# Optimization experiments

Hardware: AMD Instinct MI355X
Metric: run time of the kernel (lower is better)

The kernel has to match this reference:

```python
import math
import jax, jax.numpy as jnp
import numpy as np

B, N, D, H, PREFIX = 2, 2048, 2048, 16, 512
HD = D // H
ROPE_BASE = 10000.0

def _rope(x):
    # x: [b, h, n, d]; rotate-half RoPE with positions 0..n-1
    d = x.shape[-1]
    n = x.shape[-2]
    inv_freq = 1.0 / (ROPE_BASE ** (jnp.arange(0, d, 2, dtype=jnp.float32) / d))  # [d/2]
    pos = jnp.arange(n, dtype=jnp.float32)
    freqs = pos[:, None] * inv_freq[None, :]            # [n, d/2]
    cos, sin = jnp.cos(freqs), jnp.sin(freqs)
    x1, x2 = x[..., : d // 2], x[..., d // 2 :]
    return jnp.concatenate([x1 * cos - x2 * sin, x2 * cos + x1 * sin], axis=-1).astype(x.dtype)

def setup_inputs() -> dict:
    key = jax.random.key(0)
    ks = jax.random.split(key, 6)
    x = jax.random.normal(ks[0], (B, N, D), dtype=jnp.float32)
    prefix_k = jax.random.normal(ks[1], (B, H, PREFIX, HD), dtype=jnp.float32)
    prefix_v = jax.random.normal(ks[2], (B, H, PREFIX, HD), dtype=jnp.float32)
    Wqkv = jax.random.normal(ks[3], (D, 3 * D), dtype=jnp.float32) * (D ** -0.5)
    bqkv = jnp.zeros((3 * D,), dtype=jnp.float32)
    Wff = jax.random.normal(ks[4], (D, D), dtype=jnp.float32) * (D ** -0.5)
    bff = jnp.zeros((D,), dtype=jnp.float32)
    # causal mask over current tokens; prefix (cache) columns fully visible
    causal = jnp.tril(jnp.ones((N, N), dtype=jnp.int32))
    mask = jnp.concatenate([jnp.ones((N, PREFIX), dtype=jnp.int32), causal], axis=1)[None, None]  # [1,1,N,N+PREFIX]
    return {"x": x, "mask": mask, "prefix_k": prefix_k, "prefix_v": prefix_v,
            "Wqkv": Wqkv, "bqkv": bqkv, "Wff": Wff, "bff": bff}

def reference(x, mask, prefix_k, prefix_v, Wqkv, bqkv, Wff, bff):
    b, n, d = x.shape
    h = prefix_k.shape[1]
    hd = d // h
    qkv = (x @ Wqkv + bqkv).reshape(b, n, 3, h, hd)      # 'b n (c h d)'
    qkv = jnp.transpose(qkv, (2, 0, 3, 1, 4))            # -> c b h n d
    q, k, v = qkv[0], qkv[1], qkv[2]
    k = jnp.concatenate([prefix_k, k], axis=2)           # [b,h,kt,hd]
    v = jnp.concatenate([prefix_v, v], axis=2)
    next_prefix_kv = jnp.stack([k, v])                   # cached BEFORE rope (as in source)
    q = _rope(q)
    k = _rope(k)
    scores = jnp.einsum('bhqd,bhkd->bhqk', q, k) / math.sqrt(hd)
    scores = jnp.where(mask == 0, jnp.finfo(scores.dtype).min, scores)
    probs = jax.nn.softmax(scores, axis=-1)              # dropout_prob=0.0 -> identity
    attn_o = jnp.einsum('bhqk,bhkd->bhqd', probs, v)
    attn_o = jnp.transpose(attn_o, (0, 2, 1, 3)).reshape(b, n, d)
    return attn_o @ Wff + bff, next_prefix_kv
```

## Files before the change

kernel.cpp:

```cpp
#include <hip/hip_runtime.h>
#include <hip/hip_bf16.h>
#include <stdint.h>

#define TPB 256

using f32x4 = __attribute__((ext_vector_type(4))) float;
using s16x8 = __attribute__((ext_vector_type(8))) short;
using s16x4 = __attribute__((ext_vector_type(4))) short;

__device__ __forceinline__ short f2bf(float f){
  union { float f; uint32_t u; } v; v.f = f;
  uint32_t u = v.u;
  uint32_t r = (u + 0x7fffu + ((u >> 16) & 1u)) >> 16;
  return (short)(uint16_t)r;
}
__device__ __forceinline__ float bf2f(short b){
  union { uint32_t u; float f; } v; v.u = ((uint32_t)(uint16_t)b) << 16;
  return v.f;
}
__device__ __forceinline__ f32x4 mfma16(s16x8 a, s16x8 b, f32x4 c){
  return __builtin_amdgcn_mfma_f32_16x16x32_bf16(a, b, c, 0, 0, 0);
}

#define AS1(p) ((const __attribute__((address_space(1))) void*)(p))
#define AS3(p) ((__attribute__((address_space(3))) void*)(p))

__global__ void k_cvt_bf16(const float* __restrict__ src, short* __restrict__ dst, int n8){
  int i = blockIdx.x * TPB + threadIdx.x;
  if (i >= n8) return;
  const float4* s4 = (const float4*)src;
  float4 a = s4[2*i], b = s4[2*i+1];
  s16x8 o;
  o[0]=f2bf(a.x); o[1]=f2bf(a.y); o[2]=f2bf(a.z); o[3]=f2bf(a.w);
  o[4]=f2bf(b.x); o[5]=f2bf(b.y); o[6]=f2bf(b.z); o[7]=f2bf(b.w);
  *(s16x8*)(dst + 8*(size_t)i) = o;
}

__global__ void k_trans_cvt(const float* __restrict__ W, short* __restrict__ WT, int K, int Nn){
  __shared__ float ls[32][33];
  int k0 = blockIdx.x * 32, n0 = blockIdx.y * 32;
  int c = threadIdx.x & 31, i = threadIdx.x >> 5;
#pragma unroll
  for (int rr = 0; rr < 4; rr++){
    int row = i*4 + rr;
    ls[row][c] = W[(size_t)(k0+row)*Nn + n0 + c];
  }
  __syncthreads();
#pragma unroll
  for (int rr = 0; rr < 4; rr++){
    int ro = i*4 + rr;
    WT[(size_t)(n0+ro)*K + k0 + c] = f2bf(ls[c][ro]);
  }
}

template<int EPI>
__global__ void __launch_bounds__(512, 2) k_gemm8(
    const short* __restrict__ A, const short* __restrict__ Bt,
    int Nn, int K,
    const float* __restrict__ bias,
    float* __restrict__ outp,
    float* __restrict__ kvout,
    short* __restrict__ qpre, short* __restrict__ kpre, short* __restrict__ vpre)
{
  __shared__ __align__(16) short As[3][16384];
  __shared__ __align__(16) short Bs[3][8192];
  const int tid = threadIdx.x;
  const int w = tid >> 6, l = tid & 63;
  const int lrow = l & 15, lg = l >> 4;
  const int wm = w >> 1, wn = w & 1;
  const int m0 = blockIdx.x << 8, n0 = blockIdx.y << 7;
  const int NT = K >> 6;

  f32x4 acc[4][4] = {};

#define STAGE_A(slot, t, j) do {                                             \
    int chunk = ((w*4 + (j)) << 6) + l;                                      \
    int row = chunk >> 3, cc = chunk & 7;                                    \
    __builtin_amdgcn_global_load_lds(                                        \
      AS1(A + (size_t)(m0+row)*K + (t)*64 + ((cc ^ (row&7)) << 3)),          \
      AS3(&As[slot][(w*4 + (j)) << 9]), 16, 0, 0);                           \
  } while(0)
#define STAGE_B(slot, t, j) do {                                             \
    int chunk = ((w*2 + (j)) << 6) + l;                                      \
    int row = chunk >> 3, cc = chunk & 7;                                    \
    __builtin_amdgcn_global_load_lds(                                        \
      AS1(Bt + (size_t)(n0+row)*K + (t)*64 + ((cc ^ (row&7)) << 3)),         \
      AS3(&Bs[slot][(w*2 + (j)) << 9]), 16, 0, 0);                           \
  } while(0)

  STAGE_A(0,0,0); STAGE_A(0,0,1); STAGE_A(0,0,2); STAGE_A(0,0,3);
  STAGE_B(0,0,0); STAGE_B(0,0,1);
  STAGE_A(1,1,0); STAGE_A(1,1,1); STAGE_A(1,1,2); STAGE_A(1,1,3);
  STAGE_B(1,1,0); STAGE_B(1,1,1);

  int slot = 0;
  for (int t = 0; t < NT; ++t){
    if (t < NT-1) asm volatile("s_waitcnt vmcnt(6)" ::: "memory");
    else          asm volatile("s_waitcnt vmcnt(0)" ::: "memory");
    __builtin_amdgcn_s_barrier();
    asm volatile("" ::: "memory");
    const int sslot = (slot == 0) ? 2 : slot - 1;
    const bool st = (t+2) < NT;
    const char* ab = (const char*)As[slot];
    const char* bb = (const char*)Bs[slot];

    s16x8 bfr[4][2];
#pragma unroll
    for (int ni = 0; ni < 4; ni++){
      int row = wn*64 + ni*16 + lrow;
#pragma unroll
      for (int ks = 0; ks < 2; ks++)
        bfr[ni][ks] = *(const s16x8*)(bb + row*128 + ((ks*64 + lg*16) ^ ((row&7)<<4)));
    }
    s16x8 af[2][2];
#pragma unroll
    for (int mi = 0; mi < 2; mi++){
      int row = wm*64 + mi*16 + lrow;
#pragma unroll
      for (int ks = 0; ks < 2; ks++)
        af[mi][ks] = *(const s16x8*)(ab + row*128 + ((ks*64 + lg*16) ^ ((row&7)<<4)));
    }
    if (st){ STAGE_A(sslot,t+2,0); STAGE_A(sslot,t+2,1); STAGE_B(sslot,t+2,0); }
    __builtin_amdgcn_s_setprio(1);
#pragma unroll
    for (int ks = 0; ks < 2; ks++)
#pragma unroll
      for (int mi = 0; mi < 2; mi++)
#pragma unroll
        for (int ni = 0; ni < 4; ni++)
          acc[mi][ni] = mfma16(af[mi][ks], bfr[ni][ks], acc[mi][ni]);
    __builtin_amdgcn_s_setprio(0);
    asm volatile("" ::: "memory");
    __builtin_amdgcn_s_barrier();
    asm volatile("" ::: "memory");

    s16x8 af2[2][2];
#pragma unroll
    for (int mi = 0; mi < 2; mi++){
      int row = wm*64 + (mi+2)*16 + lrow;
#pragma unroll
      for (int ks = 0; ks < 2; ks++)
        af2[mi][ks] = *(const s16x8*)(ab + row*128 + ((ks*64 + lg*16) ^ ((row&7)<<4)));
    }
    if (st){ STAGE_A(sslot,t+2,2); STAGE_A(sslot,t+2,3); STAGE_B(sslot,t+2,1); }
    __builtin_amdgcn_s_setprio(1);
#pragma unroll
    for (int ks = 0; ks < 2; ks++)
#pragma unroll
      for (int mi = 0; mi < 2; mi++)
#pragma unroll
        for (int ni = 0; ni < 4; ni++)
          acc[mi+2][ni] = mfma16(af2[mi][ks], bfr[ni][ks], acc[mi+2][ni]);
    __builtin_amdgcn_s_setprio(0);
    slot = (slot == 2) ? 0 : slot + 1;
  }
#undef STAGE_A
#undef STAGE_B

#pragma unroll
  for (int mi = 0; mi < 4; mi++){
#pragma unroll
    for (int ni = 0; ni < 4; ni++){
      const int c  = n0 + wn*64 + ni*16 + lrow;
      const int mb = m0 + wm*64 + mi*16 + lg*4;
      const float bv = bias[c];
      if (EPI == 1){
#pragma unroll
        for (int r = 0; r < 4; r++)
          outp[(size_t)(mb+r)*Nn + c] = acc[mi][ni][r] + bv;
      } else {
        const int s = c >> 11, h = (c >> 7) & 15, tt = c & 127;
#pragma unroll
        for (int r = 0; r < 4; r++){
          const int m = mb + r;
          const int b = m >> 11, n = m & 2047;
          const int bh = b*16 + h;
          const float val = acc[mi][ni][r] + bv;
          if (s == 0){
            qpre[((size_t)bh*2048 + n)*128 + tt] = f2bf(val);
          } else if (s == 1){
            kvout[((size_t)bh*2560 + 512 + n)*128 + tt] = val;
            kpre[((size_t)bh*2048 + n)*128 + tt] = f2bf(val);
          } else {
            kvout[(size_t)(32 + bh)*327680 + (size_t)(512 + n)*128 + tt] = val;
            vpre[((size_t)bh*2048 + n)*128 + tt] = f2bf(val);
          }
        }
      }
    }
  }
}

__global__ void k_rope_k_new(const short* __restrict__ kpre, short* __restrict__ kr){
  int gid = blockIdx.x * TPB + threadIdx.x;
  int jb = (gid & 7) * 8; size_t row = gid >> 3;
  int bh = (int)(row >> 11), n = (int)(row & 2047);
  int pos = 512 + n;
  s16x8 v1 = *(const s16x8*)&kpre[row*128 + jb];
  s16x8 v2 = *(const s16x8*)&kpre[row*128 + 64 + jb];
  s16x8 o1, o2;
#pragma unroll
  for (int e = 0; e < 8; e++){
    float invf = __expf((float)(jb + e) * (-9.210340371976184f/64.0f));
    float sn, cs; __sincosf((float)pos * invf, &sn, &cs);
    float x1 = bf2f(v1[e]), x2 = bf2f(v2[e]);
    o1[e] = f2bf(x1*cs - x2*sn);
    o2[e] = f2bf(x2*cs + x1*sn);
  }
  size_t drow = (size_t)bh*2560 + pos;
  *(s16x8*)&kr[drow*128 + jb]      = o1;
  *(s16x8*)&kr[drow*128 + 64 + jb] = o2;
}

__global__ void k_rope_k_prefix(const float* __restrict__ pk, float* __restrict__ kvout0,
                                short* __restrict__ kr){
  int gid = blockIdx.x * TPB + threadIdx.x;
  int jb = (gid & 7) * 8; size_t row = gid >> 3;
  int bh = (int)(row >> 9), p = (int)(row & 511);
  float4 a1 = *(const float4*)&pk[row*128 + jb];
  float4 a2 = *(const float4*)&pk[row*128 + jb + 4];
  float4 b1 = *(const float4*)&pk[row*128 + 64 + jb];
  float4 b2 = *(const float4*)&pk[row*128 + 64 + jb + 4];
  size_t orow = (size_t)bh*2560 + p;
  *(float4*)&kvout0[orow*128 + jb]          = a1;
  *(float4*)&kvout0[orow*128 + jb + 4]      = a2;
  *(float4*)&kvout0[orow*128 + 64 + jb]     = b1;
  *(float4*)&kvout0[orow*128 + 64 + jb + 4] = b2;
  float x1[8] = {a1.x,a1.y,a1.z,a1.w,a2.x,a2.y,a2.z,a2.w};
  float x2[8] = {b1.x,b1.y,b1.z,b1.w,b2.x,b2.y,b2.z,b2.w};
  s16x8 o1, o2;
#pragma unroll
  for (int e = 0; e < 8; e++){
    float invf = __expf((float)(jb + e) * (-9.210340371976184f/64.0f));
    float sn, cs; __sincosf((float)p * invf, &sn, &cs);
    o1[e] = f2bf(x1[e]*cs - x2[e]*sn);
    o2[e] = f2bf(x2[e]*cs + x1[e]*sn);
  }
  *(s16x8*)&kr[orow*128 + jb]      = o1;
  *(s16x8*)&kr[orow*128 + 64 + jb] = o2;
}

__global__ void k_v_prefix(const float* __restrict__ pv, float* __restrict__ kvout1,
                           short* __restrict__ vT){
  __shared__ float ls[32][129];
  int bh = blockIdx.x >> 4, pt = blockIdx.x & 15;
  int p0 = pt*32, tid = threadIdx.x;
#pragma unroll
  for (int i = 0; i < 16; i++){
    int idx = i*TPB + tid; int p = idx >> 7, t = idx & 127;
    float v = pv[((size_t)bh*512 + p0 + p)*128 + t];
    ls[p][t] = v;
    kvout1[((size_t)bh*2560 + p0 + p)*128 + t] = v;
  }
  __syncthreads();
#pragma unroll
  for (int i = 0; i < 16; i++){
    int idx = i*TPB + tid; int t = idx >> 5, p = idx & 31;
    vT[((size_t)bh*128 + t)*2560 + p0 + p] = f2bf(ls[p][t]);
  }
}

__global__ void k_v_new(const short* __restrict__ vpre, short* __restrict__ vT){
  __shared__ float ls[32][129];
  int bh = blockIdx.x >> 6, nt = blockIdx.x & 63;
  int n0 = nt*32, tid = threadIdx.x;
#pragma unroll
  for (int i = 0; i < 16; i++){
    int idx = i*TPB + tid; int p = idx >> 7, t = idx & 127;
    ls[p][t] = bf2f(vpre[((size_t)bh*2048 + n0 + p)*128 + t]);
  }
  __syncthreads();
#pragma unroll
  for (int i = 0; i < 16; i++){
    int idx = i*TPB + tid; int t = idx >> 5, p = idx & 31;
    vT[((size_t)bh*128 + t)*2560 + 512 + n0 + p] = f2bf(ls[p][t]);
  }
}

__global__ void __launch_bounds__(256, 2) k_attn(
    const short* __restrict__ qr, const short* __restrict__ kr,
    const short* __restrict__ vT, short* __restrict__ attno)
{
  __shared__ short Ks[2][64*128];
  __shared__ short VTs[2][128*64];
  __shared__ short Ps[4][32*64];
  const int bh = blockIdx.x;
  const int qt = 15 - (int)blockIdx.y;
  const int n = 10 + 2*qt;
  const int tid = threadIdx.x, w = tid >> 6, l = tid & 63;
  const int lrow = l & 15, lg = l >> 4;
  const int b = bh >> 4, h = bh & 15;
  const int qbw = qt*128 + w*32;

  s16x8 qf[2][4];
  {
    const float sc = 0.088388347648318447f;
#pragma unroll
    for (int qb = 0; qb < 2; qb++){
      const int nr = qbw + qb*16 + lrow;
      const size_t rr = (size_t)bh*2048 + nr;
#pragma unroll
      for (int ks = 0; ks < 4; ks++)
        qf[qb][ks] = *(const s16x8*)&qr[rr*128 + ks*32 + lg*8];
#pragma unroll
      for (int ks = 0; ks < 2; ks++){
#pragma unroll
        for (int e = 0; e < 8; e++){
          const int j = ks*32 + lg*8 + e;
          const float invf = __expf((float)j * (-9.210340371976184f/64.0f));
          float sn, cs;
          __sincosf((float)nr * invf, &sn, &cs);
          float x1 = bf2f(qf[qb][ks][e]), x2 = bf2f(qf[qb][ks+2][e]);
          qf[qb][ks][e]   = f2bf((x1*cs - x2*sn) * sc);
          qf[qb][ks+2][e] = f2bf((x2*cs + x1*sn) * sc);
        }
      }
    }
  }

#define STAGE_KV(buf, kv0s) do {                                                    \
    _Pragma("unroll")                                                               \
    for (int i_ = 0; i_ < 4; i_++){                                                 \
      int chunk = i_*256 + tid;                                                     \
      int row = chunk >> 4, cc = (chunk & 15) ^ (row & 7);                          \
      __builtin_amdgcn_global_load_lds(                                             \
        AS1(kr + ((size_t)bh*2560 + (kv0s) + row)*128 + cc*8),                      \
        AS3((char*)Ks[buf] + (i_*256 + w*64)*16), 16, 0, 0);                        \
    }                                                                               \
    _Pragma("unroll")                                                               \
    for (int i_ = 0; i_ < 4; i_++){                                                 \
      int chunk = i_*256 + tid;                                                     \
      int row = chunk >> 3, cc = (chunk & 7) ^ (row & 7);                           \
      __builtin_amdgcn_global_load_lds(                                             \
        AS1(vT + ((size_t)bh*128 + row)*2560 + (kv0s) + cc*8),                      \
        AS3((char*)VTs[buf] + (i_*256 + w*64)*16), 16, 0, 0);                       \
    }                                                                               \
  } while(0)

  STAGE_KV(0, 0);
  STAGE_KV(1, 64);

  char* psw = (char*)&Ps[w][0];
  f32x4 acc0[8] = {}, acc1[8] = {};
  float mr0 = -1e30f, ls0 = 0.f;
  float mr1 = -1e30f, ls1 = 0.f;

  for (int t = 0; t < n; t++){
    if (t+1 < n) asm volatile("s_waitcnt vmcnt(8)" ::: "memory");
    else         asm volatile("s_waitcnt vmcnt(0)" ::: "memory");
    __builtin_amdgcn_s_barrier();
    asm volatile("" ::: "memory");
    const char* kb_ = (const char*)Ks[t&1];
    const char* vb_ = (const char*)VTs[t&1];
    const int kv0 = t*64;

    f32x4 sf0[4], sf1[4];
    __builtin_amdgcn_s_setprio(1);
#pragma unroll
    for (int kb = 0; kb < 4; kb++){
      f32x4 s0 = {0.f,0.f,0.f,0.f}, s1 = {0.f,0.f,0.f,0.f};
#pragma unroll
      for (int ks = 0; ks < 4; ks++){
        int row  = kb*16 + lrow;
        int colb = ks*64 + lg*16;
        s16x8 kf = *(const s16x8*)(kb_ + row*256 + (colb ^ ((row&7)<<4)));
        s0 = mfma16(kf, qf[0][ks], s0);
        s1 = mfma16(kf, qf[1][ks], s1);
      }
      sf0[kb] = s0; sf1[kb] = s1;
    }
    __builtin_amdgcn_s_setprio(0);

    if (kv0 + 63 > 512 + qbw){
      const int qme0 = 512 + qbw + lrow;
      const int qme1 = qme0 + 16;
#pragma unroll
      for (int kb = 0; kb < 4; kb++)
#pragma unroll
        for (int r = 0; r < 4; r++){
          int kg = kv0 + kb*16 + lg*4 + r;
          if (kg > qme0) sf0[kb][r] = -1e30f;
          if (kg > qme1) sf1[kb][r] = -1e30f;
        }
    }

    {
      float m_ = fmaxf(
          fmaxf(fmaxf(fmaxf(sf0[0][0],sf0[0][1]),fmaxf(sf0[0][2],sf0[0][3])),
                fmaxf(fmaxf(sf0[1][0],sf0[1][1]),fmaxf(sf0[1][2],sf0[1][3]))),
          fmaxf(fmaxf(fmaxf(sf0[2][0],sf0[2][1]),fmaxf(sf0[2][2],sf0[2][3])),
                fmaxf(fmaxf(sf0[3][0],sf0[3][1]),fmaxf(sf0[3][2],sf0[3][3]))));
      m_ = fmaxf(m_, __shfl_xor(m_, 16));
      m_ = fmaxf(m_, __shfl_xor(m_, 32));
      if (__any(m_ > mr0 + 8.f)){
        float mnew = fmaxf(mr0, m_);
        float sc = __expf(mr0 - mnew);
        mr0 = mnew; ls0 *= sc;
        float scr[4];
#pragma unroll
        for (int r = 0; r < 4; r++)
          scr[r] = __shfl(sc, (l & 48) | (lg*4 + r));
#pragma unroll
        for (int dt = 0; dt < 8; dt++)
#pragma unroll
          for (int r = 0; r < 4; r++) acc0[dt][r] *= scr[r];
      }
#pragma unroll
      for (int kb = 0; kb < 4; kb++){
        float p0 = __expf(sf0[kb][0] - mr0);
        float p1 = __expf(sf0[kb][1] - mr0);
        float p2 = __expf(sf0[kb][2] - mr0);
        float p3 = __expf(sf0[kb][3] - mr0);
        ls0 += (p0+p1)+(p2+p3);
        s16x4 pk4 = { f2bf(p0), f2bf(p1), f2bf(p2), f2bf(p3) };
        *(s16x4*)(psw + (lrow*128 + ((kb*32 + lg*8) ^ ((lrow&7)<<4)))) = pk4;
      }
    }
    {
      float m_ = fmaxf(
          fmaxf(fmaxf(fmaxf(sf1[0][0],sf1[0][1]),fmaxf(sf1[0][2],sf1[0][3])),
                fmaxf(fmaxf(sf1[1][0],sf1[1][1]),fmaxf(sf1[1][2],sf1[1][3]))),
          fmaxf(fmaxf(fmaxf(sf1[2][0],sf1[2][1]),fmaxf(sf1[2][2],sf1[2][3])),
                fmaxf(fmaxf(sf1[3][0],sf1[3][1]),fmaxf(sf1[3][2],sf1[3][3]))));
      m_ = fmaxf(m_, __shfl_xor(m_, 16));
      m_ = fmaxf(m_, __shfl_xor(m_, 32));
      if (__any(m_ > mr1 + 8.f)){
        float mnew = fmaxf(mr1, m_);
        float sc = __expf(mr1 - mnew);
        mr1 = mnew; ls1 *= sc;
        float scr[4];
#pragma unroll
        for (int r = 0; r < 4; r++)
          scr[r] = __shfl(sc, (l & 48) | (lg*4 + r));
#pragma unroll
        for (int dt = 0; dt < 8; dt++)
#pragma unroll
          for (int r = 0; r < 4; r++) acc1[dt][r] *= scr[r];
      }
#pragma unroll
      for (int kb = 0; kb < 4; kb++){
        float p0 = __expf(sf1[kb][0] - mr1);
        float p1 = __expf(sf1[kb][1] - mr1);
        float p2 = __expf(sf1[kb][2] - mr1);
        float p3 = __expf(sf1[kb][3] - mr1);
        ls1 += (p0+p1)+(p2+p3);
        s16x4 pk4 = { f2bf(p0), f2bf(p1), f2bf(p2), f2bf(p3) };
        *(s16x4*)(psw + ((16 + lrow)*128 + ((kb*32 + lg*8) ^ ((lrow&7)<<4)))) = pk4;
      }
    }

    __builtin_amdgcn_s_setprio(1);
#pragma unroll
    for (int kp = 0; kp < 2; kp++){
      s16x8 pa0 = *(const s16x8*)(psw + (lrow*128       + ((kp*64 + lg*16) ^ ((lrow&7)<<4))));
      s16x8 pa1 = *(const s16x8*)(psw + ((16+lrow)*128  + ((kp*64 + lg*16) ^ ((lrow&7)<<4))));
#pragma unroll
      for (int dt = 0; dt < 8; dt++){
        int vrow = dt*16 + lrow;
        int vcolb = kp*64 + lg*16;
        s16x8 vf = *(const s16x8*)(vb_ + vrow*128 + (vcolb ^ ((vrow&7)<<4)));
        acc0[dt] = mfma16(pa0, vf, acc0[dt]);
        acc1[dt] = mfma16(pa1, vf, acc1[dt]);
      }
    }
    __builtin_amdgcn_s_setprio(0);

    asm volatile("" ::: "memory");
    __builtin_amdgcn_s_barrier();
    asm volatile("" ::: "memory");
    if (t + 2 < n) STAGE_KV(t&1, (t+2)*64);
  }

  float lsa = ls0;
  lsa += __shfl_xor(lsa, 16);
  lsa += __shfl_xor(lsa, 32);
  float lsb = ls1;
  lsb += __shfl_xor(lsb, 16);
  lsb += __shfl_xor(lsb, 32);
  float linv0[4], linv1[4];
#pragma unroll
  for (int r = 0; r < 4; r++){
    linv0[r] = 1.f / __shfl(lsa, (l & 48) | (lg*4 + r));
    linv1[r] = 1.f / __shfl(lsb, (l & 48) | (lg*4 + r));
  }
#pragma unroll
  for (int dt = 0; dt < 8; dt++){
#pragma unroll
    for (int r = 0; r < 4; r++){
      const int dcol = h*128 + dt*16 + lrow;
      const int nrow0 = qbw + lg*4 + r;
      const int nrow1 = qbw + 16 + lg*4 + r;
      attno[((size_t)b*2048 + nrow0)*2048 + dcol] = f2bf(acc0[dt][r] * linv0[r]);
      attno[((size_t)b*2048 + nrow1)*2048 + dcol] = f2bf(acc1[dt][r] * linv1[r]);
    }
  }
#undef STAGE_KV
}

extern "C" void kernel_launch(void* const* d_in, const int* in_sizes, int n_in,
                              void* d_out, int out_size, void* d_ws, size_t ws_size,
                              hipStream_t stream)
{
  const float* x    = (const float*)d_in[0];
  const float* pk   = (const float*)d_in[2];
  const float* pv   = (const float*)d_in[3];
  const float* Wqkv = (const float*)d_in[4];
  const float* bqkv = (const float*)d_in[5];
  const float* Wff  = (const float*)d_in[6];
  const float* bff  = (const float*)d_in[7];
  float* out   = (float*)d_out;
  float* kvout = out + 8388608;

  char* ws = (char*)d_ws;
  short* xb    = (short*)(ws);
  short* wqkvT = (short*)(ws + 16777216);
  short* wffT  = (short*)(ws + 41943040);
  short* qpre  = (short*)(ws + 50331648);
  short* kpre  = (short*)(ws + 67108864);
  short* vpre  = (short*)(ws + 83886080);
  short* krp   = (short*)(ws + 117440512);
  short* vTp   = (short*)(ws + 138412032);
  short* attno = (short*)(ws + 159383552);

  k_cvt_bf16<<<4096, TPB, 0, stream>>>(x, xb, 1048576);
  k_trans_cvt<<<dim3(64, 192), TPB, 0, stream>>>(Wqkv, wqkvT, 2048, 6144);
  k_trans_cvt<<<dim3(64, 64),  TPB, 0, stream>>>(Wff,  wffT,  2048, 2048);

  k_gemm8<0><<<dim3(16, 48), 512, 0, stream>>>(xb, wqkvT, 6144, 2048, bqkv,
                                               nullptr, kvout, qpre, kpre, vpre);

  k_rope_k_new<<<2048, TPB, 0, stream>>>(kpre, krp);
  k_rope_k_prefix<<<512, TPB, 0, stream>>>(pk, kvout, krp);
  k_v_prefix<<<512, TPB, 0, stream>>>(pv, kvout + (size_t)32*327680, vTp);
  k_v_new<<<2048, TPB, 0, stream>>>(vpre, vTp);

  k_attn<<<dim3(32, 16), 256, 0, stream>>>(qpre, krp, vTp, attno);

  k_gemm8<1><<<dim3(16, 16), 512, 0, stream>>>(attno, wffT, 2048, 2048, bff,
                                               out, nullptr, nullptr, nullptr, nullptr);
}
```

Before: 306.8 us.

## Split softmax P writes into two halves interleaved with PV MFMAs, halving P LDS

```diff
diff --git a/kernel.cpp b/kernel.cpp
--- a/kernel.cpp
+++ b/kernel.cpp
@@ -283,7 +283,7 @@
 {
   __shared__ short Ks[2][64*128];
   __shared__ short VTs[2][128*64];
-  __shared__ short Ps[4][32*64];
+  __shared__ short Ps[4][32*32];
   const int bh = blockIdx.x;
   const int qt = 15 - (int)blockIdx.y;
   const int n = 10 + 2*qt;
@@ -341,6 +341,7 @@
   STAGE_KV(1, 64);
 
   char* psw = (char*)&Ps[w][0];
+  const int pswz = (lrow & 3) << 4;
   f32x4 acc0[8] = {}, acc1[8] = {};
   float mr0 = -1e30f, ls0 = 0.f;
   float mr1 = -1e30f, ls1 = 0.f;
@@ -405,16 +406,6 @@
 #pragma unroll
           for (int r = 0; r < 4; r++) acc0[dt][r] *= scr[r];
       }
-#pragma unroll
-      for (int kb = 0; kb < 4; kb++){
-        float p0 = __expf(sf0[kb][0] - mr0);
-        float p1 = __expf(sf0[kb][1] - mr0);
-        float p2 = __expf(sf0[kb][2] - mr0);
-        float p3 = __expf(sf0[kb][3] - mr0);
-        ls0 += (p0+p1)+(p2+p3);
-        s16x4 pk4 = { f2bf(p0), f2bf(p1), f2bf(p2), f2bf(p3) };
-        *(s16x4*)(psw + (lrow*128 + ((kb*32 + lg*8) ^ ((lrow&7)<<4)))) = pk4;
-      }
     }
     {
       float m_ = fmaxf(
@@ -437,27 +428,65 @@
 #pragma unroll
           for (int r = 0; r < 4; r++) acc1[dt][r] *= scr[r];
       }
-#pragma unroll
-      for (int kb = 0; kb < 4; kb++){
-        float p0 = __expf(sf1[kb][0] - mr1);
-        float p1 = __expf(sf1[kb][1] - mr1);
-        float p2 = __expf(sf1[kb][2] - mr1);
-        float p3 = __expf(sf1[kb][3] - mr1);
-        ls1 += (p0+p1)+(p2+p3);
-        s16x4 pk4 = { f2bf(p0), f2bf(p1), f2bf(p2), f2bf(p3) };
-        *(s16x4*)(psw + ((16 + lrow)*128 + ((kb*32 + lg*8) ^ ((lrow&7)<<4)))) = pk4;
-      }
-    }
-
+    }
+
+#pragma unroll
+    for (int kb = 0; kb < 2; kb++){
+      float p0 = __expf(sf0[kb][0] - mr0);
+      float p1 = __expf(sf0[kb][1] - mr0);
+      float p2 = __expf(sf0[kb][2] - mr0);
+      float p3 = __expf(sf0[kb][3] - mr0);
+      ls0 += (p0+p1)+(p2+p3);
+      s16x4 pk4 = { f2bf(p0), f2bf(p1), f2bf(p2), f2bf(p3) };
+      *(s16x4*)(psw + lrow*64 + ((kb*32 + lg*8) ^ pswz)) = pk4;
+      float q0 = __expf(sf1[kb][0] - mr1);
+      float q1 = __expf(sf1[kb][1] - mr1);
+      float q2 = __expf(sf1[kb][2] - mr1);
+      float q3 = __expf(sf1[kb][3] - mr1);
+      ls1 += (q0+q1)+(q2+q3);
+      s16x4 qk4 = { f2bf(q0), f2bf(q1), f2bf(q2), f2bf(q3) };
+      *(s16x4*)(psw + (16+lrow)*64 + ((kb*32 + lg*8) ^ pswz)) = qk4;
+    }
     __builtin_amdgcn_s_setprio(1);
-#pragma unroll
-    for (int kp = 0; kp < 2; kp++){
-      s16x8 pa0 = *(const s16x8*)(psw + (lrow*128       + ((kp*64 + lg*16) ^ ((lrow&7)<<4))));
-      s16x8 pa1 = *(const s16x8*)(psw + ((16+lrow)*128  + ((kp*64 + lg*16) ^ ((lrow&7)<<4))));
+    {
+      s16x8 pa0 = *(const s16x8*)(psw + lrow*64      + ((lg*16) ^ pswz));
+      s16x8 pa1 = *(const s16x8*)(psw + (16+lrow)*64 + ((lg*16) ^ pswz));
 #pragma unroll
       for (int dt = 0; dt < 8; dt++){
         int vrow = dt*16 + lrow;
-        int vcolb = kp*64 + lg*16;
+        int vcolb = lg*16;
+        s16x8 vf = *(const s16x8*)(vb_ + vrow*128 + (vcolb ^ ((vrow&7)<<4)));
+        acc0[dt] = mfma16(pa0, vf, acc0[dt]);
+        acc1[dt] = mfma16(pa1, vf, acc1[dt]);
+      }
+    }
+    __builtin_amdgcn_s_setprio(0);
+
+#pragma unroll
+    for (int kb = 2; kb < 4; kb++){
+      float p0 = __expf(sf0[kb][0] - mr0);
+      float p1 = __expf(sf0[kb][1] - mr0);
+      float p2 = __expf(sf0[kb][2] - mr0);
+      float p3 = __expf(sf0[kb][3] - mr0);
+      ls0 += (p0+p1)+(p2+p3);
+      s16x4 pk4 = { f2bf(p0), f2bf(p1), f2bf(p2), f2bf(p3) };
+      *(s16x4*)(psw + lrow*64 + (((kb&1)*32 + lg*8) ^ pswz)) = pk4;
+      float q0 = __expf(sf1[kb][0] - mr1);
+      float q1 = __expf(sf1[kb][1] - mr1);
+      float q2 = __expf(sf1[kb][2] - mr1);
+      float q3 = __expf(sf1[kb][3] - mr1);
+      ls1 += (q0+q1)+(q2+q3);
+      s16x4 qk4 = { f2bf(q0), f2bf(q1), f2bf(q2), f2bf(q3) };
+      *(s16x4*)(psw + (16+lrow)*64 + (((kb&1)*32 + lg*8) ^ pswz)) = qk4;
+    }
+    __builtin_amdgcn_s_setprio(1);
+    {
+      s16x8 pa0 = *(const s16x8*)(psw + lrow*64      + ((lg*16) ^ pswz));
+      s16x8 pa1 = *(const s16x8*)(psw + (16+lrow)*64 + ((lg*16) ^ pswz));
+#pragma unroll
+      for (int dt = 0; dt < 8; dt++){
+        int vrow = dt*16 + lrow;
+        int vcolb = 64 + lg*16;
         s16x8 vf = *(const s16x8*)(vb_ + vrow*128 + (vcolb ^ ((vrow&7)<<4)));
         acc0[dt] = mfma16(pa0, vf, acc0[dt]);
         acc1[dt] = mfma16(pa1, vf, acc1[dt]);
```

Result: no change. 311.3 us (+1.5%).
